# Kernel optimization log

Measured on AMD Instinct MI355X. Metric: run time of the kernel, lower is better.

Reference implementation:

```python
import jax, jax.numpy as jnp
import numpy as np

D_MODEL = 1024
NUM_HEADS = 16
HEAD_DIM = D_MODEL // NUM_HEADS
B, S = 4, 2048


def setup_inputs() -> dict:
    key = jax.random.key(0)
    ks = jax.random.split(key, 12)
    s = 1.0 / np.sqrt(D_MODEL)
    return {
        "inputs_q": jax.random.normal(ks[0], (B, S, D_MODEL), jnp.float32),
        "inputs_k": jax.random.normal(ks[1], (B, S, D_MODEL), jnp.float32),
        "inputs_v": jax.random.normal(ks[2], (B, S, D_MODEL), jnp.float32),
        "Wq": jax.random.normal(ks[3], (D_MODEL, D_MODEL), jnp.float32) * s,
        "bq": jax.random.normal(ks[4], (D_MODEL,), jnp.float32) * 0.01,
        "Wk": jax.random.normal(ks[5], (D_MODEL, D_MODEL), jnp.float32) * s,
        "bk": jax.random.normal(ks[6], (D_MODEL,), jnp.float32) * 0.01,
        "Wv": jax.random.normal(ks[7], (D_MODEL, D_MODEL), jnp.float32) * s,
        "bv": jax.random.normal(ks[8], (D_MODEL,), jnp.float32) * 0.01,
        "Wo": jax.random.normal(ks[9], (D_MODEL, D_MODEL), jnp.float32) * s,
        "bo": jax.random.normal(ks[10], (D_MODEL,), jnp.float32) * 0.01,
    }


def reference(inputs_q, inputs_k, inputs_v, Wq, bq, Wk, bk, Wv, bv, Wo, bo):
    b, s, _ = inputs_q.shape
    # linear projections
    q = inputs_q @ Wq + bq  # [b, s, d_model]
    k = inputs_k @ Wk + bk
    v = inputs_v @ Wv + bv
    # split heads: bsd -> bhsd
    q = q.reshape(b, s, NUM_HEADS, HEAD_DIM).transpose(0, 2, 1, 3)
    k = k.reshape(b, s, NUM_HEADS, HEAD_DIM).transpose(0, 2, 1, 3)
    v = v.reshape(b, s, NUM_HEADS, HEAD_DIM).transpose(0, 2, 1, 3)
    scale = 1.0 / jnp.sqrt(jnp.asarray(HEAD_DIM, q.dtype))
    scores = jnp.einsum('bhqd,bhkd->bhqk', q, k) * scale  # [b,h,s,s]
    # causal mask: position q attends to k <= q
    causal = jnp.tril(jnp.ones((s, s), dtype=bool))
    scores = jnp.where(causal[None, None], scores, jnp.asarray(-jnp.inf, scores.dtype))
    attn = jax.nn.softmax(scores, axis=-1)
    ctx = jnp.einsum('bhqk,bhkd->bhqd', attn, v)  # [b,h,s,hd]
    ctx = ctx.transpose(0, 2, 1, 3).reshape(b, s, D_MODEL)
    return ctx @ Wo + bo
```

## Files before the change

kernel.cpp:

```cpp
#include <hip/hip_runtime.h>
#include <math.h>
#include <type_traits>

typedef __bf16 bf16;
typedef __attribute__((ext_vector_type(8))) __bf16 bf16x8;
typedef __attribute__((ext_vector_type(4))) float f32x4;
typedef __attribute__((ext_vector_type(16))) float f32x16;

#define SEQ 2048
#define DM 1024
#define NH 16
#define HD 64
#define BATCH 4

#define NEG_BIG (-1e30f)
#define SCALE_L2E 0.18033688011f

__device__ inline bf16x8 cvt_f32x8(const float* p) {
  f32x4 x0 = *(const f32x4*)p;
  f32x4 x1 = *(const f32x4*)(p + 4);
  bf16x8 r;
  r[0] = (bf16)x0[0]; r[1] = (bf16)x0[1]; r[2] = (bf16)x0[2]; r[3] = (bf16)x0[3];
  r[4] = (bf16)x1[0]; r[5] = (bf16)x1[1]; r[6] = (bf16)x1[2]; r[7] = (bf16)x1[3];
  return r;
}

__device__ inline void async_copy16(const bf16* g, bf16* l) {
  __builtin_amdgcn_global_load_lds(
      (const __attribute__((address_space(1))) unsigned int*)g,
      (__attribute__((address_space(3))) unsigned int*)l, 16, 0, 0);
}

__global__ __launch_bounds__(256) void cvt_kernel(const float* __restrict__ src,
                                                  bf16* __restrict__ dst) {
  size_t i = ((size_t)blockIdx.x * 256 + threadIdx.x) * 8;
  *(bf16x8*)(dst + i) = cvt_f32x8(src + i);
}

__global__ __launch_bounds__(256) void transpose_w_kernel(
    const float* __restrict__ Wq, const float* __restrict__ Wk,
    const float* __restrict__ Wv, const float* __restrict__ Wo,
    bf16* __restrict__ Tq, bf16* __restrict__ Tk,
    bf16* __restrict__ Tv, bf16* __restrict__ To) {
  __shared__ bf16 tile[64 * 66];
  int z = blockIdx.z;
  const float* src = (z == 0) ? Wq : (z == 1) ? Wk : (z == 2) ? Wv : Wo;
  bf16* dst = (z == 0) ? Tq : (z == 1) ? Tk : (z == 2) ? Tv : To;
  int n0 = blockIdx.x * 64, k0 = blockIdx.y * 64;
  int t = threadIdx.x;
  int c = t & 63, rr = t >> 6;
#pragma unroll
  for (int i = 0; i < 16; i++) {
    int k = i * 4 + rr;
    tile[k * 66 + c] = (bf16)src[(size_t)(k0 + k) * DM + n0 + c];
  }
  __syncthreads();
#pragma unroll
  for (int i = 0; i < 16; i++) {
    int n = i * 4 + rr;
    dst[(size_t)(n0 + n) * DM + k0 + c] = tile[c * 66 + n];
  }
}

__global__ __launch_bounds__(256) void transpose_v_kernel(
    const bf16* __restrict__ Vc, bf16* __restrict__ Vt) {
  __shared__ bf16 tile[64 * 66];
  int s0 = blockIdx.x * 64;
  int bh = blockIdx.y;
  int t = threadIdx.x;
  int c = t & 63, rr = t >> 6;
  const bf16* src = Vc + (size_t)bh * SEQ * HD;
  bf16* dst = Vt + (size_t)bh * HD * SEQ;
#pragma unroll
  for (int i = 0; i < 16; i++) {
    int s = i * 4 + rr;
    tile[s * 66 + c] = src[(size_t)(s0 + s) * HD + c];
  }
  __syncthreads();
#pragma unroll
  for (int i = 0; i < 16; i++) {
    int d = i * 4 + rr;
    dst[(size_t)d * SEQ + s0 + c] = tile[c * 66 + d];
  }
}

template <typename CT, int MODE>
__global__ __launch_bounds__(256) void gemm_bias_kernel(
    const bf16* __restrict__ A, const bf16* __restrict__ Bt,
    const float* __restrict__ bias, CT* __restrict__ C) {
  __shared__ bf16 As[128 * 32];
  __shared__ bf16 Bs[128 * 32];
  int m0 = blockIdx.x * 128, n0 = blockIdx.y * 128;
  int t = threadIdx.x;
  int wave = t >> 6, lane = t & 63, lr = lane & 15, lq = lane >> 4;
  int wm = (wave & 1) * 64, wn = (wave >> 1) * 64;

  f32x4 acc[4][4];
#pragma unroll
  for (int i = 0; i < 4; i++)
#pragma unroll
    for (int j = 0; j < 4; j++) acc[i][j] = (f32x4){0.f, 0.f, 0.f, 0.f};

  int srow = wave * 32 + (lane >> 2);
  int skc = lane & 3;
  const bf16* gA0 = A + (size_t)(m0 + srow) * DM + skc * 8;
  const bf16* gA1 = gA0 + (size_t)16 * DM;
  const bf16* gB0 = Bt + (size_t)(n0 + srow) * DM + skc * 8;
  const bf16* gB1 = gB0 + (size_t)16 * DM;
  bf16* lA0 = &As[(wave * 128) * 8];
  bf16* lA1 = &As[(wave * 128 + 64) * 8];
  bf16* lB0 = &Bs[(wave * 128) * 8];
  bf16* lB1 = &Bs[(wave * 128 + 64) * 8];

  for (int k0 = 0; k0 < DM; k0 += 32) {
    async_copy16(gA0, lA0);
    async_copy16(gA1, lA1);
    async_copy16(gB0, lB0);
    async_copy16(gB1, lB1);
    gA0 += 32; gA1 += 32; gB0 += 32; gB1 += 32;
    __syncthreads();

    bf16x8 af[4], bfr[4];
#pragma unroll
    for (int i = 0; i < 4; i++)
      af[i] = *(const bf16x8*)&As[(wm + i * 16 + lr) * 32 + lq * 8];
#pragma unroll
    for (int j = 0; j < 4; j++)
      bfr[j] = *(const bf16x8*)&Bs[(wn + j * 16 + lr) * 32 + lq * 8];
#pragma unroll
    for (int i = 0; i < 4; i++)
#pragma unroll
      for (int j = 0; j < 4; j++)
        acc[i][j] = __builtin_amdgcn_mfma_f32_16x16x32_bf16(af[i], bfr[j],
                                                            acc[i][j], 0, 0, 0);
    __syncthreads();
  }

#pragma unroll
  for (int j = 0; j < 4; j++) {
    int col = n0 + wn + j * 16 + lr;
    float bv = bias[col];
#pragma unroll
    for (int i = 0; i < 4; i++) {
      int row0 = m0 + wm + i * 16 + lq * 4;
#pragma unroll
      for (int r = 0; r < 4; r++) {
        int row = row0 + r;
        float v = acc[i][j][r] + bv;
        if constexpr (MODE == 0) {
          C[(size_t)row * DM + col] = (CT)v;
        } else {
          int b = row >> 11, s = row & 2047, h = col >> 6, d = col & 63;
          C[((size_t)(b * NH + h) * SEQ + s) * HD + d] = (CT)v;
        }
      }
    }
  }
}

__global__ __launch_bounds__(256, 2) void attention_kernel(
    const bf16* __restrict__ Qc, const bf16* __restrict__ Kc,
    const bf16* __restrict__ Vt, bf16* __restrict__ ctx) {
  int h = blockIdx.y, b = blockIdx.z;
  int t = threadIdx.x, wave = t >> 6, lane = t & 63;
  int l31 = lane & 31, hh = lane >> 5;
  int p = blockIdx.x * 4 + wave;

  const bf16* Qb = Qc + (size_t)(b * NH + h) * SEQ * HD;
  const bf16* Kb = Kc + (size_t)(b * NH + h) * SEQ * HD;
  const bf16* Vb = Vt + (size_t)(b * NH + h) * HD * SEQ;
  bf16* Cb = ctx + (size_t)b * SEQ * DM + h * HD;

#pragma unroll 1
  for (int pass = 0; pass < 2; pass++) {
    int tq = pass ? (63 - p) : p;
    int q0 = tq * 32;

    bf16x8 qf[4];
#pragma unroll
    for (int st = 0; st < 4; st++)
      qf[st] = *(const bf16x8*)&Qb[(size_t)(q0 + l31) * HD + st * 16 + hh * 8];

    f32x16 o[2];
#pragma unroll
    for (int dt = 0; dt < 2; dt++)
#pragma unroll
      for (int r = 0; r < 16; r++) o[dt][r] = 0.f;
    float m_st = NEG_BIG, l_st = 0.f;

    int nch = (tq >> 1) + 1;
#pragma unroll 1
    for (int c = 0; c < nch; c++) {
      int kv0 = c * 64;
      bf16x8 kf[2][4];
#pragma unroll
      for (int kt = 0; kt < 2; kt++)
#pragma unroll
        for (int st = 0; st < 4; st++)
          kf[kt][st] = *(const bf16x8*)&Kb[(size_t)(kv0 + kt * 32 + l31) * HD +
                                           st * 16 + hh * 8];
      bf16x8 vf[2][4];
#pragma unroll
      for (int dt = 0; dt < 2; dt++)
#pragma unroll
        for (int ks = 0; ks < 4; ks++)
          vf[dt][ks] = *(const bf16x8*)&Vb[(size_t)(dt * 32 + l31) * SEQ + kv0 +
                                           ks * 16 + hh * 8];

      f32x16 s[2];
#pragma unroll
      for (int kt = 0; kt < 2; kt++) {
        f32x16 acc;
#pragma unroll
        for (int r = 0; r < 16; r++) acc[r] = 0.f;
#pragma unroll
        for (int st = 0; st < 4; st++)
          acc = __builtin_amdgcn_mfma_f32_32x32x16_bf16(kf[kt][st], qf[st],
                                                        acc, 0, 0, 0);
        s[kt] = acc;
      }

      bool diag = (c == nch - 1);
      if (diag) {
        int q_g = q0 + l31;
#pragma unroll
        for (int kt = 0; kt < 2; kt++)
#pragma unroll
          for (int r = 0; r < 16; r++) {
            int key = kv0 + kt * 32 + (r & 3) + 8 * (r >> 2) + 4 * hh;
            float v = s[kt][r] * SCALE_L2E;
            s[kt][r] = (key > q_g) ? NEG_BIG : v;
          }
      } else {
#pragma unroll
        for (int kt = 0; kt < 2; kt++)
#pragma unroll
          for (int r = 0; r < 16; r++) s[kt][r] *= SCALE_L2E;
      }

      float mx = s[0][0];
#pragma unroll
      for (int r = 1; r < 16; r++) mx = fmaxf(mx, s[0][r]);
#pragma unroll
      for (int r = 0; r < 16; r++) mx = fmaxf(mx, s[1][r]);
      mx = fmaxf(mx, __shfl_xor(mx, 32));
      float mnew = fmaxf(m_st, mx);
      float alpha = exp2f(m_st - mnew);
      m_st = mnew;
      float rs = 0.f;
#pragma unroll
      for (int kt = 0; kt < 2; kt++)
#pragma unroll
        for (int r = 0; r < 16; r++) {
          float pv = exp2f(s[kt][r] - mnew);
          s[kt][r] = pv;
          rs += pv;
        }
      rs += __shfl_xor(rs, 32);
      l_st = l_st * alpha + rs;
#pragma unroll
      for (int dt = 0; dt < 2; dt++)
#pragma unroll
        for (int r = 0; r < 16; r++) o[dt][r] *= alpha;

      unsigned int W[2][8];
#pragma unroll
      for (int kt = 0; kt < 2; kt++)
#pragma unroll
        for (int w = 0; w < 8; w++) {
          unsigned int u;
          asm("v_cvt_pk_bf16_f32 %0, %1, %2"
              : "=v"(u)
              : "v"(s[kt][2 * w]), "v"(s[kt][2 * w + 1]));
          W[kt][w] = u;
        }
      bf16x8 pf[4];
#pragma unroll
      for (int kt = 0; kt < 2; kt++) {
        unsigned int x1 = hh ? W[kt][0] : W[kt][2];
        unsigned int x2 = hh ? W[kt][1] : W[kt][3];
        unsigned int x3 = hh ? W[kt][4] : W[kt][6];
        unsigned int x4 = hh ? W[kt][5] : W[kt][7];
        unsigned int y1 = (unsigned int)__shfl_xor((int)x1, 32);
        unsigned int y2 = (unsigned int)__shfl_xor((int)x2, 32);
        unsigned int y3 = (unsigned int)__shfl_xor((int)x3, 32);
        unsigned int y4 = (unsigned int)__shfl_xor((int)x4, 32);
        unsigned int* f0 = (unsigned int*)&pf[2 * kt];
        unsigned int* f1 = (unsigned int*)&pf[2 * kt + 1];
        f0[0] = hh ? y1 : W[kt][0];
        f0[1] = hh ? y2 : W[kt][1];
        f0[2] = hh ? W[kt][2] : y1;
        f0[3] = hh ? W[kt][3] : y2;
        f1[0] = hh ? y3 : W[kt][4];
        f1[1] = hh ? y4 : W[kt][5];
        f1[2] = hh ? W[kt][6] : y3;
        f1[3] = hh ? W[kt][7] : y4;
      }

#pragma unroll
      for (int dt = 0; dt < 2; dt++)
#pragma unroll
        for (int ks = 0; ks < 4; ks++)
          o[dt] = __builtin_amdgcn_mfma_f32_32x32x16_bf16(vf[dt][ks], pf[ks],
                                                          o[dt], 0, 0, 0);
    }

    float inv = 1.f / l_st;
    int row = q0 + l31;
#pragma unroll
    for (int dt = 0; dt < 2; dt++)
#pragma unroll
      for (int r = 0; r < 16; r += 2) {
        float va = o[dt][r] * inv;
        float vb = o[dt][r + 1] * inv;
        unsigned int u;
        asm("v_cvt_pk_bf16_f32 %0, %1, %2" : "=v"(u) : "v"(va), "v"(vb));
        int d = dt * 32 + (r & 3) + 8 * (r >> 2) + 4 * hh;
        *(unsigned int*)&Cb[(size_t)row * DM + d] = u;
      }
  }
}

extern "C" void kernel_launch(void* const* d_in, const int* in_sizes, int n_in,
                              void* d_out, int out_size, void* d_ws,
                              size_t ws_size, hipStream_t stream) {
  const float* iq = (const float*)d_in[0];
  const float* ik = (const float*)d_in[1];
  const float* iv = (const float*)d_in[2];
  const float* Wq = (const float*)d_in[3];
  const float* bq = (const float*)d_in[4];
  const float* Wk = (const float*)d_in[5];
  const float* bk = (const float*)d_in[6];
  const float* Wv = (const float*)d_in[7];
  const float* bv = (const float*)d_in[8];
  const float* Wo = (const float*)d_in[9];
  const float* bo = (const float*)d_in[10];

  char* ws = (char*)d_ws;
  const size_t MB = 1024 * 1024;
  bf16* Tq = (bf16*)(ws + 0 * MB);
  bf16* Tk = (bf16*)(ws + 2 * MB);
  bf16* Tv = (bf16*)(ws + 4 * MB);
  bf16* To = (bf16*)(ws + 6 * MB);
  bf16* Qc = (bf16*)(ws + 8 * MB);
  bf16* Kc = (bf16*)(ws + 24 * MB);
  bf16* Vc = (bf16*)(ws + 40 * MB);
  bf16* X = (bf16*)d_out;
  bf16* Vtp = (bf16*)d_out;
  bf16* Cx = Vc;

  transpose_w_kernel<<<dim3(16, 16, 4), 256, 0, stream>>>(Wq, Wk, Wv, Wo, Tq,
                                                          Tk, Tv, To);
  cvt_kernel<<<dim3(4096), 256, 0, stream>>>(iq, X);
  gemm_bias_kernel<bf16, 1><<<dim3(64, 8), 256, 0, stream>>>(X, Tq, bq, Qc);
  cvt_kernel<<<dim3(4096), 256, 0, stream>>>(ik, X);
  gemm_bias_kernel<bf16, 1><<<dim3(64, 8), 256, 0, stream>>>(X, Tk, bk, Kc);
  cvt_kernel<<<dim3(4096), 256, 0, stream>>>(iv, X);
  gemm_bias_kernel<bf16, 1><<<dim3(64, 8), 256, 0, stream>>>(X, Tv, bv, Vc);
  transpose_v_kernel<<<dim3(32, 64), 256, 0, stream>>>(Vc, Vtp);
  attention_kernel<<<dim3(8, 16, 4), 256, 0, stream>>>(Qc, Kc, Vtp, Cx);
  gemm_bias_kernel<float, 0><<<dim3(64, 8), 256, 0, stream>>>(Cx, To, bo,
                                                              (float*)d_out);
}
```

Before: 401.3 us.

## Split attention KV range across wave pairs with LDS merge and XCD-aware block mapping

Result: no change. 405.0 us (+0.9%).

```diff
diff --git a/kernel.cpp b/kernel.cpp
--- a/kernel.cpp
+++ b/kernel.cpp
@@ -161,158 +161,184 @@
 __global__ __launch_bounds__(256, 2) void attention_kernel(
     const bf16* __restrict__ Qc, const bf16* __restrict__ Kc,
     const bf16* __restrict__ Vt, bf16* __restrict__ ctx) {
-  int h = blockIdx.y, b = blockIdx.z;
+  __shared__ float ls_o[2][2][16][64];
+  __shared__ float ls_ml[2][2][64];
+
   int t = threadIdx.x, wave = t >> 6, lane = t & 63;
   int l31 = lane & 31, hh = lane >> 5;
-  int p = blockIdx.x * 4 + wave;
+  int pair = wave >> 1, sub = wave & 1;
+
+  int bid = blockIdx.x;
+  int xcd = bid & 7, qq = bid >> 3;
+  int g = xcd + 8 * (qq & 7);
+  int bx = qq >> 3;
+  int h = g & 15, b = g >> 4;
+
+  int tq = pair ? (63 - bx) : bx;
+  int q0 = tq * 32;
+  int nch = (tq >> 1) + 1;
+  int c0 = sub ? (nch >> 1) : 0;
+  int c1 = sub ? nch : (nch >> 1);
 
   const bf16* Qb = Qc + (size_t)(b * NH + h) * SEQ * HD;
   const bf16* Kb = Kc + (size_t)(b * NH + h) * SEQ * HD;
   const bf16* Vb = Vt + (size_t)(b * NH + h) * HD * SEQ;
   bf16* Cb = ctx + (size_t)b * SEQ * DM + h * HD;
 
+  bf16x8 qf[4];
+#pragma unroll
+  for (int st = 0; st < 4; st++)
+    qf[st] = *(const bf16x8*)&Qb[(size_t)(q0 + l31) * HD + st * 16 + hh * 8];
+
+  f32x16 o[2];
+#pragma unroll
+  for (int dt = 0; dt < 2; dt++)
+#pragma unroll
+    for (int r = 0; r < 16; r++) o[dt][r] = 0.f;
+  float m_st = NEG_BIG, l_st = 0.f;
+
 #pragma unroll 1
-  for (int pass = 0; pass < 2; pass++) {
-    int tq = pass ? (63 - p) : p;
-    int q0 = tq * 32;
-
-    bf16x8 qf[4];
-#pragma unroll
-    for (int st = 0; st < 4; st++)
-      qf[st] = *(const bf16x8*)&Qb[(size_t)(q0 + l31) * HD + st * 16 + hh * 8];
-
-    f32x16 o[2];
-#pragma unroll
-    for (int dt = 0; dt < 2; dt++)
-#pragma unroll
-      for (int r = 0; r < 16; r++) o[dt][r] = 0.f;
-    float m_st = NEG_BIG, l_st = 0.f;
-
-    int nch = (tq >> 1) + 1;
-#pragma unroll 1
-    for (int c = 0; c < nch; c++) {
-      int kv0 = c * 64;
-      bf16x8 kf[2][4];
+  for (int c = c0; c < c1; c++) {
+    int kv0 = c * 64;
+    bf16x8 kf[2][4];
+#pragma unroll
+    for (int kt = 0; kt < 2; kt++)
+#pragma unroll
+      for (int st = 0; st < 4; st++)
+        kf[kt][st] = *(const bf16x8*)&Kb[(size_t)(kv0 + kt * 32 + l31) * HD +
+                                         st * 16 + hh * 8];
+    bf16x8 vf[2][4];
+#pragma unroll
+    for (int dt = 0; dt < 2; dt++)
+#pragma unroll
+      for (int ks = 0; ks < 4; ks++)
+        vf[dt][ks] = *(const bf16x8*)&Vb[(size_t)(dt * 32 + l31) * SEQ + kv0 +
+                                         ks * 16 + hh * 8];
+
+    f32x16 s[2];
+    __builtin_amdgcn_s_setprio(1);
+#pragma unroll
+    for (int kt = 0; kt < 2; kt++) {
+      f32x16 acc;
+#pragma unroll
+      for (int r = 0; r < 16; r++) acc[r] = 0.f;
+#pragma unroll
+      for (int st = 0; st < 4; st++)
+        acc = __builtin_amdgcn_mfma_f32_32x32x16_bf16(kf[kt][st], qf[st], acc,
+                                                      0, 0, 0);
+      s[kt] = acc;
+    }
+    __builtin_amdgcn_s_setprio(0);
+
+    bool diag = (c == nch - 1);
+    if (diag) {
+      int q_g = q0 + l31;
 #pragma unroll
       for (int kt = 0; kt < 2; kt++)
 #pragma unroll
-        for (int st = 0; st < 4; st++)
-          kf[kt][st] = *(const bf16x8*)&Kb[(size_t)(kv0 + kt * 32 + l31) * HD +
-                                           st * 16 + hh * 8];
-      bf16x8 vf[2][4];
-#pragma unroll
-      for (int dt = 0; dt < 2; dt++)
-#pragma unroll
-        for (int ks = 0; ks < 4; ks++)
-          vf[dt][ks] = *(const bf16x8*)&Vb[(size_t)(dt * 32 + l31) * SEQ + kv0 +
-                                           ks * 16 + hh * 8];
-
-      f32x16 s[2];
-#pragma unroll
-      for (int kt = 0; kt < 2; kt++) {
-        f32x16 acc;
-#pragma unroll
-        for (int r = 0; r < 16; r++) acc[r] = 0.f;
-#pragma unroll
-        for (int st = 0; st < 4; st++)
-          acc = __builtin_amdgcn_mfma_f32_32x32x16_bf16(kf[kt][st], qf[st],
-                                                        acc, 0, 0, 0);
-        s[kt] = acc;
+        for (int r = 0; r < 16; r++) {
+          int key = kv0 + kt * 32 + (r & 3) + 8 * (r >> 2) + 4 * hh;
+          float v = s[kt][r] * SCALE_L2E;
+          s[kt][r] = (key > q_g) ? NEG_BIG : v;
+        }
+    } else {
+#pragma unroll
+      for (int kt = 0; kt < 2; kt++)
+#pragma unroll
+        for (int r = 0; r < 16; r++) s[kt][r] *= SCALE_L2E;
+    }
+
+    float mx = s[0][0];
+#pragma unroll
+    for (int r = 1; r < 16; r++) mx = fmaxf(mx, s[0][r]);
+#pragma unroll
+    for (int r = 0; r < 16; r++) mx = fmaxf(mx, s[1][r]);
+    mx = fmaxf(mx, __shfl_xor(mx, 32));
+    float mnew = fmaxf(m_st, mx);
+    float alpha = exp2f(m_st - mnew);
+    m_st = mnew;
+    float rs = 0.f;
+#pragma unroll
+    for (int kt = 0; kt < 2; kt++)
+#pragma unroll
+      for (int r = 0; r < 16; r++) {
+        float pv = exp2f(s[kt][r] - mnew);
+        s[kt][r] = pv;
+        rs += pv;
       }
-
-      bool diag = (c == nch - 1);
-      if (diag) {
-        int q_g = q0 + l31;
-#pragma unroll
-        for (int kt = 0; kt < 2; kt++)
-#pragma unroll
-          for (int r = 0; r < 16; r++) {
-            int key = kv0 + kt * 32 + (r & 3) + 8 * (r >> 2) + 4 * hh;
-            float v = s[kt][r] * SCALE_L2E;
-            s[kt][r] = (key > q_g) ? NEG_BIG : v;
-          }
-      } else {
-#pragma unroll
-        for (int kt = 0; kt < 2; kt++)
-#pragma unroll
-          for (int r = 0; r < 16; r++) s[kt][r] *= SCALE_L2E;
+    rs += __shfl_xor(rs, 32);
+    l_st = l_st * alpha + rs;
+#pragma unroll
+    for (int dt = 0; dt < 2; dt++)
+#pragma unroll
+      for (int r = 0; r < 16; r++) o[dt][r] *= alpha;
+
+    unsigned int W[2][8];
+#pragma unroll
+    for (int kt = 0; kt < 2; kt++)
+#pragma unroll
+      for (int w = 0; w < 8; w++) {
+        unsigned int u;
+        asm("v_cvt_pk_bf16_f32 %0, %1, %2"
+            : "=v"(u)
+            : "v"(s[kt][2 * w]), "v"(s[kt][2 * w + 1]));
+        W[kt][w] = u;
       }
-
-      float mx = s[0][0];
-#pragma unroll
-      for (int r = 1; r < 16; r++) mx = fmaxf(mx, s[0][r]);
-#pragma unroll
-      for (int r = 0; r < 16; r++) mx = fmaxf(mx, s[1][r]);
-      mx = fmaxf(mx, __shfl_xor(mx, 32));
-      float mnew = fmaxf(m_st, mx);
-      float alpha = exp2f(m_st - mnew);
-      m_st = mnew;
-      float rs = 0.f;
-#pragma unroll
-      for (int kt = 0; kt < 2; kt++)
-#pragma unroll
-        for (int r = 0; r < 16; r++) {
-          float pv = exp2f(s[kt][r] - mnew);
-          s[kt][r] = pv;
-          rs += pv;
-        }
-      rs += __shfl_xor(rs, 32);
-      l_st = l_st * alpha + rs;
-#pragma unroll
-      for (int dt = 0; dt < 2; dt++)
-#pragma unroll
-        for (int r = 0; r < 16; r++) o[dt][r] *= alpha;
-
-      unsigned int W[2][8];
-#pragma unroll
-      for (int kt = 0; kt < 2; kt++)
-#pragma unroll
-        for (int w = 0; w < 8; w++) {
-          unsigned int u;
-          asm("v_cvt_pk_bf16_f32 %0, %1, %2"
-              : "=v"(u)
-              : "v"(s[kt][2 * w]), "v"(s[kt][2 * w + 1]));
-          W[kt][w] = u;
-        }
-      bf16x8 pf[4];
-#pragma unroll
-      for (int kt = 0; kt < 2; kt++) {
-        unsigned int x1 = hh ? W[kt][0] : W[kt][2];
-        unsigned int x2 = hh ? W[kt][1] : W[kt][3];
-        unsigned int x3 = hh ? W[kt][4] : W[kt][6];
-        unsigned int x4 = hh ? W[kt][5] : W[kt][7];
-        unsigned int y1 = (unsigned int)__shfl_xor((int)x1, 32);
-        unsigned int y2 = (unsigned int)__shfl_xor((int)x2, 32);
-        unsigned int y3 = (unsigned int)__shfl_xor((int)x3, 32);
-        unsigned int y4 = (unsigned int)__shfl_xor((int)x4, 32);
-        unsigned int* f0 = (unsigned int*)&pf[2 * kt];
-        unsigned int* f1 = (unsigned int*)&pf[2 * kt + 1];
-        f0[0] = hh ? y1 : W[kt][0];
-        f0[1] = hh ? y2 : W[kt][1];
-        f0[2] = hh ? W[kt][2] : y1;
-        f0[3] = hh ? W[kt][3] : y2;
-        f1[0] = hh ? y3 : W[kt][4];
-        f1[1] = hh ? y4 : W[kt][5];
-        f1[2] = hh ? W[kt][6] : y3;
-        f1[3] = hh ? W[kt][7] : y4;
-      }
-
-#pragma unroll
-      for (int dt = 0; dt < 2; dt++)
-#pragma unroll
-        for (int ks = 0; ks < 4; ks++)
-          o[dt] = __builtin_amdgcn_mfma_f32_32x32x16_bf16(vf[dt][ks], pf[ks],
-                                                          o[dt], 0, 0, 0);
+    bf16x8 pf[4];
+#pragma unroll
+    for (int kt = 0; kt < 2; kt++) {
+      unsigned int x1 = hh ? W[kt][0] : W[kt][2];
+      unsigned int x2 = hh ? W[kt][1] : W[kt][3];
+      unsigned int x3 = hh ? W[kt][4] : W[kt][6];
+      unsigned int x4 = hh ? W[kt][5] : W[kt][7];
+      unsigned int y1 = (unsigned int)__shfl_xor((int)x1, 32);
+      unsigned int y2 = (unsigned int)__shfl_xor((int)x2, 32);
+      unsigned int y3 = (unsigned int)__shfl_xor((int)x3, 32);
+      unsigned int y4 = (unsigned int)__shfl_xor((int)x4, 32);
+      unsigned int* f0 = (unsigned int*)&pf[2 * kt];
+      unsigned int* f1 = (unsigned int*)&pf[2 * kt + 1];
+      f0[0] = hh ? y1 : W[kt][0];
+      f0[1] = hh ? y2 : W[kt][1];
+      f0[2] = hh ? W[kt][2] : y1;
+      f0[3] = hh ? W[kt][3] : y2;
+      f1[0] = hh ? y3 : W[kt][4];
+      f1[1] = hh ? y4 : W[kt][5];
+      f1[2] = hh ? W[kt][6] : y3;
+      f1[3] = hh ? W[kt][7] : y4;
     }
 
-    float inv = 1.f / l_st;
+    __builtin_amdgcn_s_setprio(1);
+#pragma unroll
+    for (int dt = 0; dt < 2; dt++)
+#pragma unroll
+      for (int ks = 0; ks < 4; ks++)
+        o[dt] = __builtin_amdgcn_mfma_f32_32x32x16_bf16(vf[dt][ks], pf[ks],
+                                                        o[dt], 0, 0, 0);
+    __builtin_amdgcn_s_setprio(0);
+  }
+
+  if (sub) {
+#pragma unroll
+    for (int dt = 0; dt < 2; dt++)
+#pragma unroll
+      for (int r = 0; r < 16; r++) ls_o[pair][dt][r][lane] = o[dt][r];
+    ls_ml[pair][0][lane] = m_st;
+    ls_ml[pair][1][lane] = l_st;
+  }
+  __syncthreads();
+  if (!sub) {
+    float m2 = ls_ml[pair][0][lane], l2 = ls_ml[pair][1][lane];
+    float m = fmaxf(m_st, m2);
+    float a1 = exp2f(m_st - m), a2 = exp2f(m2 - m);
+    float linv = 1.f / (l_st * a1 + l2 * a2);
     int row = q0 + l31;
 #pragma unroll
     for (int dt = 0; dt < 2; dt++)
 #pragma unroll
       for (int r = 0; r < 16; r += 2) {
-        float va = o[dt][r] * inv;
-        float vb = o[dt][r + 1] * inv;
+        float va = (o[dt][r] * a1 + ls_o[pair][dt][r][lane] * a2) * linv;
+        float vb =
+            (o[dt][r + 1] * a1 + ls_o[pair][dt][r + 1][lane] * a2) * linv;
         unsigned int u;
         asm("v_cvt_pk_bf16_f32 %0, %1, %2" : "=v"(u) : "v"(va), "v"(vb));
         int d = dt * 32 + (r & 3) + 8 * (r >> 2) + 4 * hh;
@@ -358,7 +384,7 @@
   cvt_kernel<<<dim3(4096), 256, 0, stream>>>(iv, X);
   gemm_bias_kernel<bf16, 1><<<dim3(64, 8), 256, 0, stream>>>(X, Tv, bv, Vc);
   transpose_v_kernel<<<dim3(32, 64), 256, 0, stream>>>(Vc, Vtp);
-  attention_kernel<<<dim3(8, 16, 4), 256, 0, stream>>>(Qc, Kc, Vtp, Cx);
+  attention_kernel<<<dim3(2048), 256, 0, stream>>>(Qc, Kc, Vtp, Cx);
   gemm_bias_kernel<float, 0><<<dim3(64, 8), 256, 0, stream>>>(Cx, To, bo,
                                                               (float*)d_out);
 }
```
